# Kernel tuning notes

Measured on AMD Instinct MI355X. Metric: run time of the kernel, lower is better.

## Reference

```python
import jax, jax.numpy as jnp
import numpy as np

Q, M, D = 4096, 65536, 1024
TOP_K = 8
EPS = 1e-12  # torch F.normalize eps default


def _l2_normalize(x, axis=-1):
    # matches torch.nn.functional.normalize(p=2): x / max(||x||, eps)
    norm = jnp.sqrt(jnp.sum(x * x, axis=axis, keepdims=True))
    return x / jnp.maximum(norm, EPS)


def setup_inputs() -> dict:
    key = jax.random.key(0)
    kq, kk, kv = jax.random.split(key, 3)
    query_embeddings = jax.random.normal(kq, (Q, D), dtype=jnp.float32)
    keys = jax.random.normal(kk, (M, D), dtype=jnp.float32)
    values = jax.random.normal(kv, (M, D), dtype=jnp.float32)
    return {"query_embeddings": query_embeddings, "keys": keys, "values": values, "top_k": TOP_K}


def reference(query_embeddings, keys, values, top_k):
    # L2-normalize queries and memory keys
    q = _l2_normalize(query_embeddings, axis=1)          # [Q, D]
    k = _l2_normalize(keys, axis=1)                      # [M, D]
    # dense cosine-similarity matmul
    sims = jnp.einsum('qd,md->qm', q, k)                 # [Q, M]
    # top-k selection (sorted descending, like torch.topk)
    topk_vals, topk_idx = jax.lax.top_k(sims, top_k)     # [Q, k]
    # irregular gather of retrieved values
    retrieved = values[topk_idx]                         # [Q, k, D]
    return retrieved
```

## Files before the change

### kernel.cpp

```cpp
#include <hip/hip_runtime.h>
#include <hip/hip_bf16.h>
#include <hip/hip_fp16.h>
#include <math.h>

#define Q_N 4096
#define M_N 65536
#define D_N 1024
#define TOPK 8
#define SEGS 32
#define KPS (M_N / SEGS)
#define CANDS (SEGS * TOPK)
#define NRES 16

#define GBM 256
#define GBN 256
#define GBK 64
#define GNKT (D_N / GBK)
#define CHUNKQ 1024
#define NCHUNK (Q_N / CHUNKQ)
#define NTILES (M_N / GBM)
#define CAP 512

#define BM 128
#define BN 128
#define BK 32
#define NSUB (KPS / BN)
#define NKT (D_N / BK)
#define NSTEP (NSUB * NKT)
#define QT128 (Q_N / BM)

typedef short s16x8 __attribute__((ext_vector_type(8)));
typedef float f32x4 __attribute__((ext_vector_type(4)));

__device__ __forceinline__ bool better(float v0, int i0, float v1, int i1) {
  return (v0 > v1) || (v0 == v1 && i0 < i1);
}

__device__ __forceinline__ unsigned short f2bf(float f) {
  union { __hip_bfloat16 h; unsigned short u; } c;
  c.h = __float2bfloat16(f);
  return c.u;
}
__device__ __forceinline__ unsigned short f2h(float f) {
  union { __half h; unsigned short u; } c;
  c.h = __float2half(f);
  return c.u;
}
__device__ __forceinline__ float h2f(unsigned short u) {
  union { __half h; unsigned short u; } c;
  c.u = u;
  return __half2float(c.h);
}

__device__ __forceinline__ void gll16(void* lds, const void* g) {
  __builtin_amdgcn_global_load_lds(
      (const __attribute__((address_space(1))) unsigned int*)(uintptr_t)g,
      (__attribute__((address_space(3))) unsigned int*)(uintptr_t)lds, 16, 0, 0);
}

__global__ __launch_bounds__(256) void knorm_scale_kernel(const float* __restrict__ keys,
                                                          unsigned short* __restrict__ kb,
                                                          float* __restrict__ rnk) {
  int row = blockIdx.x;
  int tid = threadIdx.x;
  float4 v = reinterpret_cast<const float4*>(keys + (size_t)row * D_N)[tid];
  float s = v.x * v.x + v.y * v.y + v.z * v.z + v.w * v.w;
#pragma unroll
  for (int off = 32; off > 0; off >>= 1) s += __shfl_down(s, off);
  __shared__ float part[4];
  __shared__ float rs;
  int lane = tid & 63, wid = tid >> 6;
  if (lane == 0) part[wid] = s;
  __syncthreads();
  if (tid == 0) {
    float t = part[0] + part[1] + part[2] + part[3];
    rs = 1.0f / fmaxf(sqrtf(t), 1e-12f);
  }
  __syncthreads();
  float r = rs;
  ushort4 o;
  o.x = f2bf(v.x * r); o.y = f2bf(v.y * r); o.z = f2bf(v.z * r); o.w = f2bf(v.w * r);
  reinterpret_cast<ushort4*>(kb + (size_t)row * D_N)[tid] = o;
  if (tid == 0) rnk[row] = r;
}

__global__ __launch_bounds__(256) void qnorm_dual_kernel(const float* __restrict__ q,
                                                         float* __restrict__ qn,
                                                         unsigned short* __restrict__ qb) {
  int row = blockIdx.x;
  int tid = threadIdx.x;
  float4 v = reinterpret_cast<const float4*>(q + (size_t)row * D_N)[tid];
  float s = v.x * v.x + v.y * v.y + v.z * v.z + v.w * v.w;
#pragma unroll
  for (int off = 32; off > 0; off >>= 1) s += __shfl_down(s, off);
  __shared__ float part[4];
  __shared__ float rs;
  int lane = tid & 63, wid = tid >> 6;
  if (lane == 0) part[wid] = s;
  __syncthreads();
  if (tid == 0) {
    float t = part[0] + part[1] + part[2] + part[3];
    rs = 1.0f / fmaxf(sqrtf(t), 1e-12f);
  }
  __syncthreads();
  float r = rs;
  float4 o;
  o.x = v.x * r; o.y = v.y * r; o.z = v.z * r; o.w = v.w * r;
  reinterpret_cast<float4*>(qn + (size_t)row * D_N)[tid] = o;
  ushort4 ob;
  ob.x = f2bf(o.x); ob.y = f2bf(o.y); ob.z = f2bf(o.z); ob.w = f2bf(o.w);
  reinterpret_cast<ushort4*>(qb + (size_t)row * D_N)[tid] = ob;
}

__global__ __launch_bounds__(512, 2) void gemm_kernel(const unsigned short* __restrict__ qb,
                                                      const unsigned short* __restrict__ kb,
                                                      unsigned short* __restrict__ sims,
                                                      float* __restrict__ qmax,
                                                      int qchunk) {
  __shared__ __align__(16) union GSmem {
    struct {
      unsigned short A[2][GBN * GBK];
      unsigned short B[2][GBM * GBK];
    } ab;
    unsigned short S[GBN][GBM + 8];
  } smem;

  const int tid = threadIdx.x;
  const int lane = tid & 63;
  const int wid = tid >> 6;
  const int wq = wid & 3;
  const int wk = wid >> 2;

  const int bid = blockIdx.x;
  const int x = bid & 7;
  const int idx = bid >> 3;
  const int keyTile = (x << 5) + (idx >> 2);
  const int qTile = idx & 3;
  const int kbase = keyTile * GBM;
  const int qbase = qchunk * CHUNKQ + qTile * GBN;
  const int qloc0 = qTile * GBN;

  const int srow8 = lane >> 3;
  const int swz = ((lane & 7) ^ srow8) << 3;
  const unsigned short* aRow = qb + (size_t)(qbase + (wid << 5) + srow8) * D_N + swz;
  const unsigned short* bRow = kb + (size_t)(kbase + (wid << 5) + srow8) * D_N + swz;

  const int fr = lane & 15;
  const int g = lane >> 4;
  const int ph0 = ((0 + g) ^ (fr & 7)) << 3;
  const int ph1 = ((4 + g) ^ (fr & 7)) << 3;

  f32x4 acc[8][4];
#pragma unroll
  for (int m = 0; m < 8; ++m)
#pragma unroll
    for (int n = 0; n < 4; ++n) acc[m][n] = (f32x4)0.0f;

#pragma unroll
  for (int i = 0; i < 4; ++i) {
    gll16(&smem.ab.A[0][0] + (wid << 11) + (i << 9), aRow + (size_t)(i << 3) * D_N);
    gll16(&smem.ab.B[0][0] + (wid << 11) + (i << 9), bRow + (size_t)(i << 3) * D_N);
  }

#pragma unroll 1
  for (int t = 0; t < GNKT; ++t) {
    __syncthreads();
    if (t + 1 < GNKT) {
      const int k2 = (t + 1) << 6;
#pragma unroll
      for (int i = 0; i < 4; ++i) {
        gll16(&smem.ab.A[(t + 1) & 1][0] + (wid << 11) + (i << 9),
              aRow + k2 + (size_t)(i << 3) * D_N);
        gll16(&smem.ab.B[(t + 1) & 1][0] + (wid << 11) + (i << 9),
              bRow + k2 + (size_t)(i << 3) * D_N);
      }
    }
    const unsigned short* Ab = &smem.ab.A[t & 1][0];
    const unsigned short* Bb = &smem.ab.B[t & 1][0];
    {
      s16x8 bq[4], af[8];
#pragma unroll
      for (int n = 0; n < 4; ++n)
        bq[n] = *(const s16x8*)(Ab + ((wq << 6) + (n << 4) + fr) * GBK + ph0);
#pragma unroll
      for (int m = 0; m < 8; ++m)
        af[m] = *(const s16x8*)(Bb + ((wk << 7) + (m << 4) + fr) * GBK + ph0);
      __builtin_amdgcn_s_setprio(1);
#pragma unroll
      for (int m = 0; m < 8; ++m)
#pragma unroll
        for (int n = 0; n < 4; ++n)
          acc[m][n] = __builtin_amdgcn_mfma_f32_16x16x32_bf16(af[m], bq[n], acc[m][n], 0, 0, 0);
      __builtin_amdgcn_s_setprio(0);
    }
    {
      s16x8 bq[4], af[8];
#pragma unroll
      for (int n = 0; n < 4; ++n)
        bq[n] = *(const s16x8*)(Ab + ((wq << 6) + (n << 4) + fr) * GBK + ph1);
#pragma unroll
      for (int m = 0; m < 8; ++m)
        af[m] = *(const s16x8*)(Bb + ((wk << 7) + (m << 4) + fr) * GBK + ph1);
      __builtin_amdgcn_s_setprio(1);
#pragma unroll
      for (int m = 0; m < 8; ++m)
#pragma unroll
        for (int n = 0; n < 4; ++n)
          acc[m][n] = __builtin_amdgcn_mfma_f32_16x16x32_bf16(af[m], bq[n], acc[m][n], 0, 0, 0);
      __builtin_amdgcn_s_setprio(0);
    }
  }

  __syncthreads();
#pragma unroll
  for (int m = 0; m < 8; ++m)
#pragma unroll
    for (int n = 0; n < 4; ++n)
#pragma unroll
      for (int j = 0; j < 4; ++j)
        smem.S[(wq << 6) + (n << 4) + fr][(wk << 7) + (m << 4) + (g << 2) + j] =
            f2h(acc[m][n][j]);
  __syncthreads();
#pragma unroll 1
  for (int it = 0; it < 16; ++it) {
    int cid = it * 512 + tid;
    int row = cid >> 5;
    int col = (cid & 31) << 3;
    s16x8 vv = *(const s16x8*)&smem.S[row][col];
    *(s16x8*)(sims + (size_t)(qloc0 + row) * M_N + kbase + col) = vv;
  }
  if (tid < 256) {
    float mx = -1e38f;
#pragma unroll 1
    for (int k8 = 0; k8 < 32; ++k8) {
      s16x8 vv = *(const s16x8*)&smem.S[tid][k8 << 3];
#pragma unroll
      for (int e = 0; e < 8; ++e) mx = fmaxf(mx, h2f((unsigned short)vv[e]));
    }
    qmax[(size_t)(qloc0 + tid) * NTILES + keyTile] = mx;
  }
}

__global__ __launch_bounds__(256) void scan2_kernel(const unsigned short* __restrict__ sims,
                                                    const float* __restrict__ qmax,
                                                    int* __restrict__ cand_idx,
                                                    int qchunk) {
  __shared__ float bufv[4][CAP];
  __shared__ int bufi[4][CAP];
  __shared__ int tlist[4][NTILES];
  __shared__ int cnts[4];
  __shared__ int tcnts[4];

  const int tid = threadIdx.x;
  const int lane = tid & 63;
  const int wv = tid >> 6;
  const int q = blockIdx.x * 4 + wv;
  const int qg = qchunk * CHUNKQ + q;
  const unsigned short* row = sims + (size_t)q * M_N;

  if (lane == 0) { cnts[wv] = 0; tcnts[wv] = 0; }
  __syncthreads();

  float4 m4 = *reinterpret_cast<const float4*>(qmax + (size_t)q * NTILES + (lane << 2));
  float tv[4] = {m4.x, m4.y, m4.z, m4.w};
  float keep[4] = {m4.x, m4.y, m4.z, m4.w};
  float T = -1e38f;
#pragma unroll 1
  for (int j = 0; j < 16; ++j) {
    float bv = tv[0]; int bi = (lane << 2);
#pragma unroll
    for (int s = 1; s < 4; ++s)
      if (better(tv[s], (lane << 2) + s, bv, bi)) { bv = tv[s]; bi = (lane << 2) + s; }
#pragma unroll
    for (int off = 32; off > 0; off >>= 1) {
      float ov = __shfl_xor(bv, off);
      int oi = __shfl_xor(bi, off);
      if (better(ov, oi, bv, bi)) { bv = ov; bi = oi; }
    }
    T = bv;
#pragma unroll
    for (int s = 0; s < 4; ++s)
      if ((lane << 2) + s == bi) tv[s] = -1e38f;
  }

#pragma unroll
  for (int s = 0; s < 4; ++s) {
    if (keep[s] >= T) {
      int p = atomicAdd(&tcnts[wv], 1);
      tlist[wv][p] = (lane << 2) + s;
    }
  }
  int tc = tcnts[wv];

#pragma unroll 1
  for (int i = 0; i < tc; ++i) {
    int t = tlist[wv][i];
    ushort4 pk = *reinterpret_cast<const ushort4*>(row + t * GBM + (lane << 2));
    unsigned short pe[4] = {pk.x, pk.y, pk.z, pk.w};
#pragma unroll
    for (int e = 0; e < 4; ++e) {
      float v = h2f(pe[e]);
      if (v >= T) {
        int p = atomicAdd(&cnts[wv], 1);
        if (p < CAP) { bufv[wv][p] = v; bufi[wv][p] = t * GBM + (lane << 2) + e; }
      }
    }
  }
  int n = cnts[wv];
  if (n > CAP) n = CAP;

  float cv[CAP / 64];
  int ci[CAP / 64];
#pragma unroll
  for (int s = 0; s < CAP / 64; ++s) {
    int id = s * 64 + lane;
    bool ok = id < n;
    cv[s] = ok ? bufv[wv][id] : -1e38f;
    ci[s] = ok ? bufi[wv][id] : 0;
  }
#pragma unroll 1
  for (int j = 0; j < 16; ++j) {
    float bv = cv[0]; int bi = ci[0];
#pragma unroll
    for (int s = 1; s < CAP / 64; ++s)
      if (better(cv[s], ci[s], bv, bi)) { bv = cv[s]; bi = ci[s]; }
#pragma unroll
    for (int off = 32; off > 0; off >>= 1) {
      float ov = __shfl_xor(bv, off);
      int oi = __shfl_xor(bi, off);
      if (better(ov, oi, bv, bi)) { bv = ov; bi = oi; }
    }
    if (lane == 0) cand_idx[(size_t)qg * 16 + j] = bi;
#pragma unroll
    for (int s = 0; s < CAP / 64; ++s)
      if (ci[s] == bi) cv[s] = -1e38f;
  }
}

__global__ __launch_bounds__(256) void rescore_kernel(const float* __restrict__ qn,
                                                      const float* __restrict__ keys,
                                                      const float* __restrict__ values,
                                                      const float* __restrict__ rnk,
                                                      const int* __restrict__ cand_idx,
                                                      float* __restrict__ out) {
  const int q = blockIdx.x;
  const int tid = threadIdx.x;
  const int lane = tid & 63;
  const int w = tid >> 6;
  __shared__ int si[16];
  __shared__ float rsc[16];
  if (tid < 16) si[tid] = cand_idx[(size_t)q * 16 + tid];
  __syncthreads();
  const float* qrow = &qn[(size_t)q * D_N + lane * 16];
  float4 qv0 = *reinterpret_cast<const float4*>(qrow + 0);
  float4 qv1 = *reinterpret_cast<const float4*>(qrow + 4);
  float4 qv2 = *reinterpret_cast<const float4*>(qrow + 8);
  float4 qv3 = *reinterpret_cast<const float4*>(qrow + 12);
  for (int c = w; c < 16; c += 4) {
    int id = si[c];
    const float* kr = &keys[(size_t)id * D_N + lane * 16];
    float4 k0 = *reinterpret_cast<const float4*>(kr + 0);
    float4 k1 = *reinterpret_cast<const float4*>(kr + 4);
    float4 k2 = *reinterpret_cast<const float4*>(kr + 8);
    float4 k3 = *reinterpret_cast<const float4*>(kr + 12);
    float s = qv0.x * k0.x + qv0.y * k0.y + qv0.z * k0.z + qv0.w * k0.w
            + qv1.x * k1.x + qv1.y * k1.y + qv1.z * k1.z + qv1.w * k1.w
            + qv2.x * k2.x + qv2.y * k2.y + qv2.z * k2.z + qv2.w * k2.w
            + qv3.x * k3.x + qv3.y * k3.y + qv3.z * k3.z + qv3.w * k3.w;
#pragma unroll
    for (int off = 32; off > 0; off >>= 1) s += __shfl_down(s, off);
    if (lane == 0) rsc[c] = s * rnk[id];
  }
  __syncthreads();
  __shared__ int sel[TOPK];
  if (tid == 0) {
    unsigned used = 0;
    for (int j = 0; j < TOPK; ++j) {
      int best = -1;
      for (int c = 0; c < 16; ++c) {
        if ((used >> c) & 1u) continue;
        if (best < 0 || better(rsc[c], si[c], rsc[best], si[best])) best = c;
      }
      used |= 1u << best;
      sel[j] = si[best];
    }
  }
  __syncthreads();
#pragma unroll
  for (int j = 0; j < TOPK; ++j) {
    int rowi = sel[j];
    float4 v = *reinterpret_cast<const float4*>(&values[(size_t)rowi * D_N + tid * 4]);
    *reinterpret_cast<float4*>(&out[(size_t)q * (TOPK * D_N) + j * D_N + tid * 4]) = v;
  }
}

__global__ __launch_bounds__(256, 3) void simsb_kernel(const unsigned short* __restrict__ qb,
                                                       const unsigned short* __restrict__ kb,
                                                       float* __restrict__ cand_val,
                                                       int* __restrict__ cand_idx) {
  __shared__ __align__(16) union SmemU {
    struct {
      unsigned short A[3][BM * BK];
      unsigned short B[3][BN * BK];
    } ab;
    struct {
      float v[BM * 4 * TOPK];
      int i[BM * 4 * TOPK];
    } mg;
  } smem;

  const int tid = threadIdx.x;
  const int lane = tid & 63;
  const int wid = tid >> 6;

  const int orig = blockIdx.x;
  const int x = orig & 7;
  const int idx = orig >> 3;
  const int qtile = ((x >> 1) << 3) + (idx & 7);
  const int seg = ((x & 1) << 4) + (idx >> 3);
  const int qbase = qtile * BM;
  const int segBase = seg * KPS;

  const int srow = (wid << 5) + (lane >> 2);
  const int scol = (((lane & 3) ^ ((lane >> 3) & 3)) << 3);
  const unsigned short* aSeg = qb + (size_t)(qbase + srow) * D_N + scol;
  const unsigned short* bSeg = kb + (size_t)(segBase + srow) * D_N + scol;

  const int fr = lane & 15;
  const int g = lane >> 4;
  const int chunk_phys = g ^ ((fr >> 1) & 3);
  const unsigned short* rB = &smem.ab.B[0][0] + (fr << 5) + (chunk_phys << 3);
  const unsigned short* rA = &smem.ab.A[0][0] + (((wid << 5) + fr) << 5) + (chunk_phys << 3);

  float lv[2][TOPK];
  int li[2][TOPK];
#pragma unroll
  for (int n = 0; n < 2; ++n)
#pragma unroll
    for (int j = 0; j < TOPK; ++j) { lv[n][j] = -1e30f; li[n][j] = 0x7fffffff; }

  f32x4 acc[8][2];
#pragma unroll
  for (int m = 0; m < 8; ++m)
#pragma unroll
    for (int n = 0; n < 2; ++n) acc[m][n] = (f32x4)0.0f;

#pragma unroll
  for (int p = 0; p < 2; ++p) {
    const unsigned short* aS = aSeg + (p << 5);
    const unsigned short* bS = bSeg + (p << 5);
    unsigned short* Ad = &smem.ab.A[p][0] + (wid << 10);
    unsigned short* Bd = &smem.ab.B[p][0] + (wid << 10);
    gll16(Ad, aS);
    gll16(Ad + 512, aS + (size_t)16 * D_N);
    gll16(Bd, bS);
    gll16(Bd + 512, bS + (size_t)16 * D_N);
  }

  const unsigned short* aP0 = aSeg + 64;
  const unsigned short* aP1 = aP0 + (size_t)16 * D_N;
  const unsigned short* bP0 = bSeg + 64;
  const unsigned short* bP1 = bP0 + (size_t)16 * D_N;

#define SWAIT_(N) asm volatile("s_waitcnt vmcnt(" #N ")" ::: "memory")
#define SWAIT(N) SWAIT_(N)

#define FOLD(V)                                                               \
  {                                                                           \
    const int kb0 = segBase + (((V) >> 5) << 7) + (g << 2);                   \
    _Pragma("unroll")                                                         \
    for (int n = 0; n < 2; ++n)                                               \
      _Pragma("unroll")                                                       \
      for (int m = 0; m < 8; ++m) {                                           \
        float q0 = acc[m][n][0], q1 = acc[m][n][1];                           \
        float q2 = acc[m][n][2], q3 = acc[m][n][3];                           \
        acc[m][n] = (f32x4)0.0f;                                              \
        float mx = fmaxf(fmaxf(q0, q1), fmaxf(q2, q3));                       \
        const int id0 = kb0 + (m << 4);                                       \
        if (better(mx, id0, lv[n][TOPK - 1], li[n][TOPK - 1])) {              \
          float vals[4] = {q0, q1, q2, q3};                                   \
          _Pragma("unroll")                                                   \
          for (int j = 0; j < 4; ++j) {                                       \
            float val = vals[j];                                              \
            int id = id0 + j;                                                 \
            if (better(val, id, lv[n][TOPK - 1], li[n][TOPK - 1])) {          \
              float cv = val; int ci = id;                                    \
              _Pragma("unroll")                                               \
              for (int p = 0; p < TOPK; ++p) {                                \
                if (better(cv, ci, lv[n][p], li[n][p])) {                     \
                  float tv = lv[n][p]; int ti = li[n][p];                     \
                  lv[n][p] = cv; li[n][p] = ci;                               \
                  cv = tv; ci = ti;                                           \
                }                                                             \
              }                                                               \
            }                                                                 \
          }                                                                   \
        }                                                                     \
      }                                                                       \
  }

#define STEP(V, SLOT, WAITN, RESTAGE)                                         \
  {                                                                           \
    SWAIT(WAITN);                                                             \
    __builtin_amdgcn_sched_barrier(0);                                        \
    __builtin_amdgcn_s_barrier();                                             \
    __builtin_amdgcn_sched_barrier(0);                                        \
    if (RESTAGE) {                                                            \
      unsigned short* Ad = &smem.ab.A[((SLOT) + 2) % 3][0] + (wid << 10);     \
      unsigned short* Bd = &smem.ab.B[((SLOT) + 2) % 3][0] + (wid << 10);     \
      gll16(Ad, aP0);                                                         \
      gll16(Ad + 512, aP1);                                                   \
      gll16(Bd, bP0);                                                         \
      gll16(Bd + 512, bP1);                                                   \
    }                                                                         \
    {                                                                         \
      const bool wrp = (((V) & 31) == 29);                                    \
      const int dA = wrp ? -992 : 32;                                         \
      const int dB = wrp ? 130080 : 32;                                       \
      aP0 += dA; aP1 += dA; bP0 += dB; bP1 += dB;                             \
    }                                                                         \
    s16x8 af[8], bq[2];                                                       \
    _Pragma("unroll")                                                         \
    for (int m = 0; m < 8; ++m)                                               \
      af[m] = *(const s16x8*)(rB + (SLOT) * 4096 + (m << 9));                 \
    bq[0] = *(const s16x8*)(rA + (SLOT) * 4096);                              \
    bq[1] = *(const s16x8*)(rA + (SLOT) * 4096 + 512);                        \
    __builtin_amdgcn_s_setprio(1);                                            \
    _Pragma("unroll")                                                         \
    for (int m = 0; m < 8; ++m) {                                             \
      acc[m][0] = __builtin_amdgcn_mfma_f32_16x16x32_bf16(af[m], bq[0], acc[m][0], 0, 0, 0); \
      acc[m][1] = __builtin_amdgcn_mfma_f32_16x16x32_bf16(af[m], bq[1], acc[m][1], 0, 0, 0); \
    }                                                                         \
    __builtin_amdgcn_s_setprio(0);                                            \
    if (((V) & 31) == 31) FOLD(V)                                             \
  }

#pragma unroll 1
  for (int vb = 0; vb < NSTEP - 2; vb += 3) {
    STEP(vb + 0, 0, 4, 1)
    STEP(vb + 1, 1, 4, 1)
    STEP(vb + 2, 2, 4, 1)
  }
  STEP(510, 0, 4, 0)
  STEP(511, 1, 0, 0)
#undef STEP
#undef FOLD
#undef SWAIT
#undef SWAIT_

  __syncthreads();

#pragma unroll
  for (int n = 0; n < 2; ++n) {
    const int ql = (wid << 5) + (n << 4) + fr;
#pragma unroll
    for (int j = 0; j < TOPK; ++j) {
      smem.mg.v[((ql << 2) + g) * TOPK + j] = lv[n][j];
      smem.mg.i[((ql << 2) + g) * TOPK + j] = li[n][j];
    }
  }
  __syncthreads();

  if (tid < BM) {
    const int rb = tid << 5;
    int p0 = 0, p1 = 0, p2 = 0, p3 = 0;
    size_t base = (size_t)(qbase + tid) * CANDS + seg * TOPK;
#pragma unroll
    for (int j = 0; j < TOPK; ++j) {
      float v0 = smem.mg.v[rb + 0 + p0];  int i0 = smem.mg.i[rb + 0 + p0];
      float v1 = smem.mg.v[rb + 8 + p1];  int i1 = smem.mg.i[rb + 8 + p1];
      float v2 = smem.mg.v[rb + 16 + p2]; int i2 = smem.mg.i[rb + 16 + p2];
      float v3 = smem.mg.v[rb + 24 + p3]; int i3 = smem.mg.i[rb + 24 + p3];
      float bv = v0; int bi = i0; int sel = 0;
      if (better(v1, i1, bv, bi)) { bv = v1; bi = i1; sel = 1; }
      if (better(v2, i2, bv, bi)) { bv = v2; bi = i2; sel = 2; }
      if (better(v3, i3, bv, bi)) { bv = v3; bi = i3; sel = 3; }
      cand_val[base + j] = bv;
      cand_idx[base + j] = bi;
      p0 += (sel == 0); p1 += (sel == 1); p2 += (sel == 2); p3 += (sel == 3);
    }
  }
}

__global__ __launch_bounds__(256) void merge_kernel(const float* __restrict__ qn,
                                                    const float* __restrict__ keys,
                                                    const float* __restrict__ values,
                                                    const float* __restrict__ rnk,
                                                    const float* __restrict__ cand_val,
                                                    const int* __restrict__ cand_idx,
                                                    float* __restrict__ out) {
  const int q = blockIdx.x;
  const int tid = threadIdx.x;
  const int lane = tid & 63;
  const int w = tid >> 6;
  __shared__ float sv[CANDS];
  __shared__ int si[CANDS];
  sv[tid] = cand_val[(size_t)q * CANDS + tid];
  si[tid] = cand_idx[(size_t)q * CANDS + tid];
  __syncthreads();
  for (int k = 2; k <= CANDS; k <<= 1) {
    for (int j = k >> 1; j > 0; j >>= 1) {
      int ixj = tid ^ j;
      if (ixj > tid) {
        float v0 = sv[tid], v1 = sv[ixj];
        int i0 = si[tid], i1 = si[ixj];
        bool desc = ((tid & k) == 0);
        bool dosw = desc ? better(v1, i1, v0, i0) : better(v0, i0, v1, i1);
        if (dosw) { sv[tid] = v1; si[tid] = i1; sv[ixj] = v0; si[ixj] = i0; }
      }
      __syncthreads();
    }
  }
  __shared__ float rsc[NRES];
  const float* qrow = &qn[(size_t)q * D_N + lane * 16];
  float4 qv0 = *reinterpret_cast<const float4*>(qrow + 0);
  float4 qv1 = *reinterpret_cast<const float4*>(qrow + 4);
  float4 qv2 = *reinterpret_cast<const float4*>(qrow + 8);
  float4 qv3 = *reinterpret_cast<const float4*>(qrow + 12);
  for (int c = w; c < NRES; c += 4) {
    int id = si[c];
    const float* kr = &keys[(size_t)id * D_N + lane * 16];
    float4 k0 = *reinterpret_cast<const float4*>(kr + 0);
    float4 k1 = *reinterpret_cast<const float4*>(kr + 4);
    float4 k2 = *reinterpret_cast<const float4*>(kr + 8);
    float4 k3 = *reinterpret_cast<const float4*>(kr + 12);
    float s = qv0.x * k0.x + qv0.y * k0.y + qv0.z * k0.z + qv0.w * k0.w
            + qv1.x * k1.x + qv1.y * k1.y + qv1.z * k1.z + qv1.w * k1.w
            + qv2.x * k2.x + qv2.y * k2.y + qv2.z * k2.z + qv2.w * k2.w
            + qv3.x * k3.x + qv3.y * k3.y + qv3.z * k3.z + qv3.w * k3.w;
#pragma unroll
    for (int off = 32; off > 0; off >>= 1) s += __shfl_down(s, off);
    if (lane == 0) rsc[c] = s * rnk[id];
  }
  __syncthreads();
  __shared__ int sel[TOPK];
  if (tid == 0) {
    unsigned used = 0;
    for (int j = 0; j < TOPK; ++j) {
      int best = -1;
      for (int c = 0; c < NRES; ++c) {
        if ((used >> c) & 1u) continue;
        if (best < 0 || better(rsc[c], si[c], rsc[best], si[best])) best = c;
      }
      used |= 1u << best;
      sel[j] = si[best];
    }
  }
  __syncthreads();
#pragma unroll
  for (int j = 0; j < TOPK; ++j) {
    int row = sel[j];
    float4 v = *reinterpret_cast<const float4*>(&values[(size_t)row * D_N + tid * 4]);
    *reinterpret_cast<float4*>(&out[(size_t)q * (TOPK * D_N) + j * D_N + tid * 4]) = v;
  }
}

extern "C" void kernel_launch(void* const* d_in, const int* in_sizes, int n_in,
                              void* d_out, int out_size, void* d_ws, size_t ws_size,
                              hipStream_t stream) {
  const float* query  = (const float*)d_in[0];
  const float* keys   = (const float*)d_in[1];
  const float* values = (const float*)d_in[2];
  float* out = (float*)d_out;
  char* ws = (char*)d_ws;

  const size_t offQn   = 0;
  const size_t offQb   = offQn + (size_t)Q_N * D_N * 4;
  const size_t offKb   = offQb + (size_t)Q_N * D_N * 2;
  const size_t offRnk  = offKb + (size_t)M_N * D_N * 2;
  const size_t offCv   = offRnk + (size_t)M_N * 4;
  const size_t offCi   = offCv + (size_t)Q_N * CANDS * 4;
  const size_t offSims = offCi + (size_t)Q_N * CANDS * 4;
  const size_t offQmax = offSims + (size_t)CHUNKQ * M_N * 2;
  const size_t needPrimary = offQmax + (size_t)CHUNKQ * NTILES * 4;

  float* qn = (float*)(ws + offQn);
  unsigned short* qb = (unsigned short*)(ws + offQb);
  unsigned short* kb = (unsigned short*)(ws + offKb);
  float* rnk = (float*)(ws + offRnk);
  float* cand_val = (float*)(ws + offCv);
  int* cand_idx = (int*)(ws + offCi);
  unsigned short* sims = (unsigned short*)(ws + offSims);
  float* qmax = (float*)(ws + offQmax);

  hipLaunchKernelGGL(knorm_scale_kernel, dim3(M_N), dim3(256), 0, stream, keys, kb, rnk);
  hipLaunchKernelGGL(qnorm_dual_kernel, dim3(Q_N), dim3(256), 0, stream, query, qn, qb);

  if (ws_size >= needPrimary) {
    for (int c = 0; c < NCHUNK; ++c) {
      hipLaunchKernelGGL(gemm_kernel, dim3(256 * 4), dim3(512), 0, stream,
                         qb, kb, sims, qmax, c);
      hipLaunchKernelGGL(scan2_kernel, dim3(CHUNKQ / 4), dim3(256), 0, stream,
                         sims, qmax, cand_idx, c);
    }
    hipLaunchKernelGGL(rescore_kernel, dim3(Q_N), dim3(256), 0, stream,
                       qn, keys, values, rnk, cand_idx, out);
  } else {
    hipLaunchKernelGGL(simsb_kernel, dim3(QT128 * SEGS), dim3(256), 0, stream,
                       qb, kb, cand_val, cand_idx);
    hipLaunchKernelGGL(merge_kernel, dim3(Q_N), dim3(256), 0, stream,
                       qn, keys, values, rnk, cand_val, cand_idx, out);
  }
}
```

Baseline: 858.1 us.

## Restructure GEMM main loop into four-phase ping-pong schedule with interleaved staging

Rewrites the bf16 similarity GEMM inner loop so each K-step is split into four sub-tiles of MFMA work. Global-to-LDS loads for the next step are interleaved between phases, with explicit waitcnt, s_barrier and sched_barrier fences and a two-deep prefetch at startup. The aim is to overlap memory staging and LDS reads with MFMA execution and to lower register pressure from fragment loads. The cost is many more block-wide barriers per iteration, plus a reliance on hand-tuned vmcnt counts that must match the number of issued loads.

```diff
diff --git a/kernel.cpp b/kernel.cpp
--- a/kernel.cpp
+++ b/kernel.cpp
@@ -119,8 +119,8 @@
                                                       int qchunk) {
   __shared__ __align__(16) union GSmem {
     struct {
-      unsigned short A[2][GBN * GBK];
-      unsigned short B[2][GBM * GBK];
+      unsigned short A[2][GBM * GBK];
+      unsigned short B[2][GBN * GBK];
     } ab;
     unsigned short S[GBN][GBM + 8];
   } smem;
@@ -128,8 +128,8 @@
   const int tid = threadIdx.x;
   const int lane = tid & 63;
   const int wid = tid >> 6;
-  const int wq = wid & 3;
-  const int wk = wid >> 2;
+  const int wn = wid & 3;
+  const int wm = wid >> 2;
 
   const int bid = blockIdx.x;
   const int x = bid & 7;
@@ -142,13 +142,14 @@
 
   const int srow8 = lane >> 3;
   const int swz = ((lane & 7) ^ srow8) << 3;
-  const unsigned short* aRow = qb + (size_t)(qbase + (wid << 5) + srow8) * D_N + swz;
-  const unsigned short* bRow = kb + (size_t)(kbase + (wid << 5) + srow8) * D_N + swz;
+  const unsigned short* aST = kb + (size_t)(kbase + (wid << 4) + srow8) * D_N + swz;
+  const unsigned short* bST = qb + (size_t)(qbase + (wid << 4) + srow8) * D_N + swz;
 
   const int fr = lane & 15;
   const int g = lane >> 4;
-  const int ph0 = ((0 + g) ^ (fr & 7)) << 3;
-  const int ph1 = ((4 + g) ^ (fr & 7)) << 3;
+  int ck[2];
+#pragma unroll
+  for (int kk = 0; kk < 2; ++kk) ck[kk] = ((((kk << 2) + g) ^ (fr & 7)) << 3);
 
   f32x4 acc[8][4];
 #pragma unroll
@@ -156,60 +157,140 @@
 #pragma unroll
     for (int n = 0; n < 4; ++n) acc[m][n] = (f32x4)0.0f;
 
-#pragma unroll
-  for (int i = 0; i < 4; ++i) {
-    gll16(&smem.ab.A[0][0] + (wid << 11) + (i << 9), aRow + (size_t)(i << 3) * D_N);
-    gll16(&smem.ab.B[0][0] + (wid << 11) + (i << 9), bRow + (size_t)(i << 3) * D_N);
-  }
+#define STG_A(HH, TT, C)                                                      \
+  {                                                                           \
+    unsigned short* d = &smem.ab.A[C][0] + (((HH) * 128 + (wid << 4)) << 6);  \
+    const unsigned short* s = aST + (size_t)(HH) * 128 * D_N + ((TT) << 6);   \
+    gll16(d, s);                                                              \
+    gll16(d + 512, s + (size_t)8 * D_N);                                      \
+  }
+#define STG_B(HH, TT, C)                                                      \
+  {                                                                           \
+    unsigned short* d = &smem.ab.B[C][0] + (((HH) * 128 + (wid << 4)) << 6);  \
+    const unsigned short* s = bST + (size_t)(HH) * 128 * D_N + ((TT) << 6);   \
+    gll16(d, s);                                                              \
+    gll16(d + 512, s + (size_t)8 * D_N);                                      \
+  }
+
+  STG_A(0, 0, 0) STG_A(1, 0, 0) STG_B(0, 0, 0) STG_B(1, 0, 0)
+  STG_A(0, 1, 1) STG_A(1, 1, 1) STG_B(0, 1, 1) STG_B(1, 1, 1)
 
 #pragma unroll 1
   for (int t = 0; t < GNKT; ++t) {
-    __syncthreads();
-    if (t + 1 < GNKT) {
-      const int k2 = (t + 1) << 6;
-#pragma unroll
-      for (int i = 0; i < 4; ++i) {
-        gll16(&smem.ab.A[(t + 1) & 1][0] + (wid << 11) + (i << 9),
-              aRow + k2 + (size_t)(i << 3) * D_N);
-        gll16(&smem.ab.B[(t + 1) & 1][0] + (wid << 11) + (i << 9),
-              bRow + k2 + (size_t)(i << 3) * D_N);
-      }
-    }
-    const unsigned short* Ab = &smem.ab.A[t & 1][0];
-    const unsigned short* Bb = &smem.ab.B[t & 1][0];
-    {
-      s16x8 bq[4], af[8];
-#pragma unroll
-      for (int n = 0; n < 4; ++n)
-        bq[n] = *(const s16x8*)(Ab + ((wq << 6) + (n << 4) + fr) * GBK + ph0);
-#pragma unroll
-      for (int m = 0; m < 8; ++m)
-        af[m] = *(const s16x8*)(Bb + ((wk << 7) + (m << 4) + fr) * GBK + ph0);
-      __builtin_amdgcn_s_setprio(1);
-#pragma unroll
-      for (int m = 0; m < 8; ++m)
-#pragma unroll
-        for (int n = 0; n < 4; ++n)
-          acc[m][n] = __builtin_amdgcn_mfma_f32_16x16x32_bf16(af[m], bq[n], acc[m][n], 0, 0, 0);
-      __builtin_amdgcn_s_setprio(0);
-    }
-    {
-      s16x8 bq[4], af[8];
-#pragma unroll
-      for (int n = 0; n < 4; ++n)
-        bq[n] = *(const s16x8*)(Ab + ((wq << 6) + (n << 4) + fr) * GBK + ph1);
-#pragma unroll
-      for (int m = 0; m < 8; ++m)
-        af[m] = *(const s16x8*)(Bb + ((wk << 7) + (m << 4) + fr) * GBK + ph1);
-      __builtin_amdgcn_s_setprio(1);
-#pragma unroll
-      for (int m = 0; m < 8; ++m)
-#pragma unroll
-        for (int n = 0; n < 4; ++n)
-          acc[m][n] = __builtin_amdgcn_mfma_f32_16x16x32_bf16(af[m], bq[n], acc[m][n], 0, 0, 0);
-      __builtin_amdgcn_s_setprio(0);
-    }
-  }
+    if (t == 0) {
+      asm volatile("s_waitcnt vmcnt(8)" ::: "memory");
+    } else {
+      asm volatile("s_waitcnt vmcnt(0)" ::: "memory");
+    }
+    __builtin_amdgcn_sched_barrier(0);
+    __builtin_amdgcn_s_barrier();
+    __builtin_amdgcn_sched_barrier(0);
+
+    const unsigned short* Ac = &smem.ab.A[t & 1][0];
+    const unsigned short* Bc = &smem.ab.B[t & 1][0];
+    const int oc = (t & 1) ^ 1;
+    const bool dost = (t + 1) < GNKT;
+
+    s16x8 ka[4][2], qa[2][2], q2[2][2];
+
+#pragma unroll
+    for (int mf = 0; mf < 4; ++mf)
+#pragma unroll
+      for (int kk = 0; kk < 2; ++kk)
+        ka[mf][kk] = *(const s16x8*)(Ac + (((wm << 7) + (mf << 4) + fr) << 6) + ck[kk]);
+#pragma unroll
+    for (int nf = 0; nf < 2; ++nf)
+#pragma unroll
+      for (int kk = 0; kk < 2; ++kk)
+        qa[nf][kk] = *(const s16x8*)(Bc + (((wn << 6) + (nf << 4) + fr) << 6) + ck[kk]);
+    if (dost) { STG_A(0, t + 1, oc) STG_B(0, t + 1, oc) }
+    asm volatile("s_waitcnt lgkmcnt(0)" ::: "memory");
+    __builtin_amdgcn_sched_barrier(0);
+    __builtin_amdgcn_s_barrier();
+    __builtin_amdgcn_sched_barrier(0);
+    __builtin_amdgcn_s_setprio(1);
+#pragma unroll
+    for (int kk = 0; kk < 2; ++kk)
+#pragma unroll
+      for (int mf = 0; mf < 4; ++mf)
+#pragma unroll
+        for (int nf = 0; nf < 2; ++nf)
+          acc[mf][nf] = __builtin_amdgcn_mfma_f32_16x16x32_bf16(ka[mf][kk], qa[nf][kk], acc[mf][nf], 0, 0, 0);
+    __builtin_amdgcn_s_setprio(0);
+    __builtin_amdgcn_s_barrier();
+    __builtin_amdgcn_sched_barrier(0);
+
+#pragma unroll
+    for (int nf = 0; nf < 2; ++nf)
+#pragma unroll
+      for (int kk = 0; kk < 2; ++kk)
+        q2[nf][kk] = *(const s16x8*)(Bc + (((wn << 6) + 32 + (nf << 4) + fr) << 6) + ck[kk]);
+    if (dost) { STG_A(1, t + 1, oc) STG_B(1, t + 1, oc) }
+    asm volatile("s_waitcnt lgkmcnt(0)" ::: "memory");
+    __builtin_amdgcn_sched_barrier(0);
+    __builtin_amdgcn_s_barrier();
+    __builtin_amdgcn_sched_barrier(0);
+    __builtin_amdgcn_s_setprio(1);
+#pragma unroll
+    for (int kk = 0; kk < 2; ++kk)
+#pragma unroll
+      for (int mf = 0; mf < 4; ++mf)
+#pragma unroll
+        for (int nf = 0; nf < 2; ++nf)
+          acc[mf][2 + nf] = __builtin_amdgcn_mfma_f32_16x16x32_bf16(ka[mf][kk], q2[nf][kk], acc[mf][2 + nf], 0, 0, 0);
+    __builtin_amdgcn_s_setprio(0);
+    __builtin_amdgcn_s_barrier();
+    __builtin_amdgcn_sched_barrier(0);
+
+#pragma unroll
+    for (int mf = 0; mf < 4; ++mf)
+#pragma unroll
+      for (int kk = 0; kk < 2; ++kk)
+        ka[mf][kk] = *(const s16x8*)(Ac + (((wm << 7) + 64 + (mf << 4) + fr) << 6) + ck[kk]);
+#pragma unroll
+    for (int nf = 0; nf < 2; ++nf)
+#pragma unroll
+      for (int kk = 0; kk < 2; ++kk)
+        qa[nf][kk] = *(const s16x8*)(Bc + (((wn << 6) + (nf << 4) + fr) << 6) + ck[kk]);
+    asm volatile("s_waitcnt lgkmcnt(0)" ::: "memory");
+    __builtin_amdgcn_sched_barrier(0);
+    __builtin_amdgcn_s_barrier();
+    __builtin_amdgcn_sched_barrier(0);
+    __builtin_amdgcn_s_setprio(1);
+#pragma unroll
+    for (int kk = 0; kk < 2; ++kk)
+#pragma unroll
+      for (int mf = 0; mf < 4; ++mf)
+#pragma unroll
+        for (int nf = 0; nf < 2; ++nf)
+          acc[4 + mf][nf] = __builtin_amdgcn_mfma_f32_16x16x32_bf16(ka[mf][kk], qa[nf][kk], acc[4 + mf][nf], 0, 0, 0);
+    __builtin_amdgcn_s_setprio(0);
+    __builtin_amdgcn_s_barrier();
+    __builtin_amdgcn_sched_barrier(0);
+
+#pragma unroll
+    for (int nf = 0; nf < 2; ++nf)
+#pragma unroll
+      for (int kk = 0; kk < 2; ++kk)
+        q2[nf][kk] = *(const s16x8*)(Bc + (((wn << 6) + 32 + (nf << 4) + fr) << 6) + ck[kk]);
+    asm volatile("s_waitcnt lgkmcnt(0)" ::: "memory");
+    __builtin_amdgcn_sched_barrier(0);
+    __builtin_amdgcn_s_barrier();
+    __builtin_amdgcn_sched_barrier(0);
+    __builtin_amdgcn_s_setprio(1);
+#pragma unroll
+    for (int kk = 0; kk < 2; ++kk)
+#pragma unroll
+      for (int mf = 0; mf < 4; ++mf)
+#pragma unroll
+        for (int nf = 0; nf < 2; ++nf)
+          acc[4 + mf][2 + nf] = __builtin_amdgcn_mfma_f32_16x16x32_bf16(ka[mf][kk], q2[nf][kk], acc[4 + mf][2 + nf], 0, 0, 0);
+    __builtin_amdgcn_s_setprio(0);
+    __builtin_amdgcn_s_barrier();
+    __builtin_amdgcn_sched_barrier(0);
+  }
+#undef STG_A
+#undef STG_B
 
   __syncthreads();
 #pragma unroll
@@ -218,7 +299,7 @@
     for (int n = 0; n < 4; ++n)
 #pragma unroll
       for (int j = 0; j < 4; ++j)
-        smem.S[(wq << 6) + (n << 4) + fr][(wk << 7) + (m << 4) + (g << 2) + j] =
+        smem.S[(wn << 6) + (n << 4) + fr][(wm << 7) + (m << 4) + (g << 2) + j] =
             f2h(acc[m][n][j]);
   __syncthreads();
 #pragma unroll 1
```

After: 896.4 us. 1.04x slower.

## Switch GEMM main loop to triple-buffered BK=32 pipeline with interleaved loads

Applied to the files above, without the earlier changes.

Restructures the bf16 similarity GEMM main loop from a double-buffered K=64 step into a three-slot ring of K=32 tiles prefetched two steps ahead. Global-to-LDS loads for A and B are split across the two MFMA half-phases, with explicit vmcnt/lgkmcnt waits, s_barriers and sched_barriers controlling overlap. The swizzle is adapted to 32-wide rows. The aim is to hide global load latency and smooth the interleaving of LDS reads with MFMA work. In exchange it adds more barriers per K step and more hand-tuned waitcnt logic that could stall if the counts are wrong.

```diff
diff --git a/kernel.cpp b/kernel.cpp
--- a/kernel.cpp
+++ b/kernel.cpp
@@ -14,8 +14,8 @@
 
 #define GBM 256
 #define GBN 256
-#define GBK 64
-#define GNKT (D_N / GBK)
+#define GBK32 32
+#define GNT32 (D_N / GBK32)
 #define CHUNKQ 1024
 #define NCHUNK (Q_N / CHUNKQ)
 #define NTILES (M_N / GBM)
@@ -119,8 +119,8 @@
                                                       int qchunk) {
   __shared__ __align__(16) union GSmem {
     struct {
-      unsigned short A[2][GBN * GBK];
-      unsigned short B[2][GBM * GBK];
+      unsigned short A[3][GBN * GBK32];
+      unsigned short B[3][GBM * GBK32];
     } ab;
     unsigned short S[GBN][GBM + 8];
   } smem;
@@ -140,15 +140,14 @@
   const int qbase = qchunk * CHUNKQ + qTile * GBN;
   const int qloc0 = qTile * GBN;
 
-  const int srow8 = lane >> 3;
-  const int swz = ((lane & 7) ^ srow8) << 3;
-  const unsigned short* aRow = qb + (size_t)(qbase + (wid << 5) + srow8) * D_N + swz;
-  const unsigned short* bRow = kb + (size_t)(kbase + (wid << 5) + srow8) * D_N + swz;
+  const int srow16 = lane >> 2;
+  const int swz32 = (((lane & 3) ^ ((lane >> 2) & 3)) << 3);
+  const unsigned short* aRow = qb + (size_t)(qbase + (wid << 5) + srow16) * D_N + swz32;
+  const unsigned short* bRow = kb + (size_t)(kbase + (wid << 5) + srow16) * D_N + swz32;
 
   const int fr = lane & 15;
   const int g = lane >> 4;
-  const int ph0 = ((0 + g) ^ (fr & 7)) << 3;
-  const int ph1 = ((4 + g) ^ (fr & 7)) << 3;
+  const int cp = ((g ^ (fr & 3)) << 3);
 
   f32x4 acc[8][4];
 #pragma unroll
@@ -156,60 +155,86 @@
 #pragma unroll
     for (int n = 0; n < 4; ++n) acc[m][n] = (f32x4)0.0f;
 
-#pragma unroll
-  for (int i = 0; i < 4; ++i) {
-    gll16(&smem.ab.A[0][0] + (wid << 11) + (i << 9), aRow + (size_t)(i << 3) * D_N);
-    gll16(&smem.ab.B[0][0] + (wid << 11) + (i << 9), bRow + (size_t)(i << 3) * D_N);
-  }
-
+#define STG_A(TT, SL)                                                         \
+  {                                                                           \
+    unsigned short* d = &smem.ab.A[SL][0] + (wid << 10);                      \
+    const unsigned short* s = aRow + ((TT) << 5);                             \
+    gll16(d, s);                                                              \
+    gll16(d + 512, s + (size_t)16 * D_N);                                     \
+  }
+#define STG_B(TT, SL)                                                         \
+  {                                                                           \
+    unsigned short* d = &smem.ab.B[SL][0] + (wid << 10);                      \
+    const unsigned short* s = bRow + ((TT) << 5);                             \
+    gll16(d, s);                                                              \
+    gll16(d + 512, s + (size_t)16 * D_N);                                     \
+  }
+
+  STG_A(0, 0) STG_B(0, 0)
+  STG_A(1, 1) STG_B(1, 1)
+
+  int slot = 0;
 #pragma unroll 1
-  for (int t = 0; t < GNKT; ++t) {
-    __syncthreads();
-    if (t + 1 < GNKT) {
-      const int k2 = (t + 1) << 6;
-#pragma unroll
-      for (int i = 0; i < 4; ++i) {
-        gll16(&smem.ab.A[(t + 1) & 1][0] + (wid << 11) + (i << 9),
-              aRow + k2 + (size_t)(i << 3) * D_N);
-        gll16(&smem.ab.B[(t + 1) & 1][0] + (wid << 11) + (i << 9),
-              bRow + k2 + (size_t)(i << 3) * D_N);
-      }
-    }
-    const unsigned short* Ab = &smem.ab.A[t & 1][0];
-    const unsigned short* Bb = &smem.ab.B[t & 1][0];
-    {
-      s16x8 bq[4], af[8];
+  for (int t = 0; t < GNT32; ++t) {
+    if (t < GNT32 - 1) {
+      asm volatile("s_waitcnt vmcnt(4)" ::: "memory");
+    } else {
+      asm volatile("s_waitcnt vmcnt(0)" ::: "memory");
+    }
+    __builtin_amdgcn_sched_barrier(0);
+    __builtin_amdgcn_s_barrier();
+    __builtin_amdgcn_sched_barrier(0);
+
+    const unsigned short* Ac = &smem.ab.A[slot][0];
+    const unsigned short* Bc = &smem.ab.B[slot][0];
+    int nslot = slot + 2; if (nslot >= 3) nslot -= 3;
+    const bool dost = (t + 2) < GNT32;
+
+    s16x8 bq[4], af[4];
+
+#pragma unroll
+    for (int mf = 0; mf < 4; ++mf)
+      af[mf] = *(const s16x8*)(Bc + ((wk << 7) + (mf << 4) + fr) * GBK32 + cp);
+#pragma unroll
+    for (int n = 0; n < 4; ++n)
+      bq[n] = *(const s16x8*)(Ac + ((wq << 6) + (n << 4) + fr) * GBK32 + cp);
+    if (dost) STG_A(t + 2, nslot)
+    __builtin_amdgcn_s_barrier();
+    __builtin_amdgcn_sched_barrier(0);
+    asm volatile("s_waitcnt lgkmcnt(0)" ::: "memory");
+    __builtin_amdgcn_sched_barrier(0);
+    __builtin_amdgcn_s_setprio(1);
+#pragma unroll
+    for (int mf = 0; mf < 4; ++mf)
 #pragma unroll
       for (int n = 0; n < 4; ++n)
-        bq[n] = *(const s16x8*)(Ab + ((wq << 6) + (n << 4) + fr) * GBK + ph0);
-#pragma unroll
-      for (int m = 0; m < 8; ++m)
-        af[m] = *(const s16x8*)(Bb + ((wk << 7) + (m << 4) + fr) * GBK + ph0);
-      __builtin_amdgcn_s_setprio(1);
-#pragma unroll
-      for (int m = 0; m < 8; ++m)
-#pragma unroll
-        for (int n = 0; n < 4; ++n)
-          acc[m][n] = __builtin_amdgcn_mfma_f32_16x16x32_bf16(af[m], bq[n], acc[m][n], 0, 0, 0);
-      __builtin_amdgcn_s_setprio(0);
-    }
-    {
-      s16x8 bq[4], af[8];
+        acc[mf][n] = __builtin_amdgcn_mfma_f32_16x16x32_bf16(af[mf], bq[n], acc[mf][n], 0, 0, 0);
+    __builtin_amdgcn_s_setprio(0);
+    __builtin_amdgcn_s_barrier();
+    __builtin_amdgcn_sched_barrier(0);
+
+#pragma unroll
+    for (int mf = 0; mf < 4; ++mf)
+      af[mf] = *(const s16x8*)(Bc + ((wk << 7) + 64 + (mf << 4) + fr) * GBK32 + cp);
+    if (dost) STG_B(t + 2, nslot)
+    __builtin_amdgcn_s_barrier();
+    __builtin_amdgcn_sched_barrier(0);
+    asm volatile("s_waitcnt lgkmcnt(0)" ::: "memory");
+    __builtin_amdgcn_sched_barrier(0);
+    __builtin_amdgcn_s_setprio(1);
+#pragma unroll
+    for (int mf = 0; mf < 4; ++mf)
 #pragma unroll
       for (int n = 0; n < 4; ++n)
-        bq[n] = *(const s16x8*)(Ab + ((wq << 6) + (n << 4) + fr) * GBK + ph1);
-#pragma unroll
-      for (int m = 0; m < 8; ++m)
-        af[m] = *(const s16x8*)(Bb + ((wk << 7) + (m << 4) + fr) * GBK + ph1);
-      __builtin_amdgcn_s_setprio(1);
-#pragma unroll
-      for (int m = 0; m < 8; ++m)
-#pragma unroll
-        for (int n = 0; n < 4; ++n)
-          acc[m][n] = __builtin_amdgcn_mfma_f32_16x16x32_bf16(af[m], bq[n], acc[m][n], 0, 0, 0);
-      __builtin_amdgcn_s_setprio(0);
-    }
-  }
+        acc[4 + mf][n] = __builtin_amdgcn_mfma_f32_16x16x32_bf16(af[mf], bq[n], acc[4 + mf][n], 0, 0, 0);
+    __builtin_amdgcn_s_setprio(0);
+    __builtin_amdgcn_s_barrier();
+    __builtin_amdgcn_sched_barrier(0);
+
+    ++slot; if (slot == 3) slot = 0;
+  }
+#undef STG_A
+#undef STG_B
 
   __syncthreads();
 #pragma unroll
```

After: 893.0 us. 1.04x slower.
